# Optimization experiments

Hardware: AMD Instinct MI355X
Metric: run time of the kernel (lower is better)

The kernel has to match this reference:

```python
import jax, jax.numpy as jnp
import numpy as np

N = 50000      # nodes
E = 400000     # edges (before self-loops)
G = 256        # graphs in batch
H = 2          # attention heads
C = 100        # out channels per head
F_IN = 336
SLOPE = 0.2    # PyG GATConv default negative_slope


def setup_inputs() -> dict:
    key = jax.random.key(0)
    ks = jax.random.split(key, 32)
    inp = {}
    inp['x'] = jax.random.normal(ks[0], (N, F_IN), dtype=jnp.float32)
    inp['edge_index'] = jax.random.randint(ks[1], (2, E), 0, N, dtype=jnp.int32)
    inp['batch'] = jnp.sort(jax.random.randint(ks[2], (N,), 0, G, dtype=jnp.int32))
    dims = [F_IN, 200, 200, 200, 200]
    k = 3
    for i in range(5):
        d = dims[i]
        inp[f'W{i+1}'] = jax.random.normal(ks[k], (d, H * C), dtype=jnp.float32) / float(np.sqrt(d)); k += 1
        inp[f'asrc{i+1}'] = jax.random.normal(ks[k], (H, C), dtype=jnp.float32) * 0.1; k += 1
        inp[f'adst{i+1}'] = jax.random.normal(ks[k], (H, C), dtype=jnp.float32) * 0.1; k += 1
        inp[f'bc{i+1}'] = jnp.zeros((H * C,), jnp.float32)
    for i, (a, b) in enumerate([(200, 100), (100, 100), (100, 29)]):
        inp[f'lw{i+1}'] = jax.random.normal(ks[k], (a, b), dtype=jnp.float32) / float(np.sqrt(a)); k += 1
        inp[f'lb{i+1}'] = jnp.zeros((b,), jnp.float32)
    return inp


def _gat(x, src, dst, W, a_s, a_d, b):
    # PyG GATConv (concat=True): per-head linear, additive attention,
    # softmax over incoming edges per destination node, weighted sum.
    h = (x @ W).reshape(-1, H, C)                      # [N,H,C]
    es = jnp.einsum('nhc,hc->nh', h, a_s)              # [N,H] src scores
    ed = jnp.einsum('nhc,hc->nh', h, a_d)              # [N,H] dst scores
    e = jax.nn.leaky_relu(es[src] + ed[dst], SLOPE)    # [E+N,H]
    m = jax.ops.segment_max(e, dst, num_segments=N)    # per-dest max (stable softmax)
    p = jnp.exp(e - m[dst])
    s = jax.ops.segment_sum(p, dst, num_segments=N)
    alpha = p / (s[dst] + 1e-16)                       # [E+N,H]
    msg = alpha[:, :, None] * h[src]                   # [E+N,H,C]
    out = jax.ops.segment_sum(msg, dst, num_segments=N)
    return out.reshape(-1, H * C) + b


def reference(x, edge_index, batch,
              W1, asrc1, adst1, bc1, W2, asrc2, adst2, bc2,
              W3, asrc3, adst3, bc3, W4, asrc4, adst4, bc4,
              W5, asrc5, adst5, bc5,
              lw1, lb1, lw2, lb2, lw3, lb3):
    loop = jnp.arange(N, dtype=edge_index.dtype)       # self-loops (PyG default)
    src = jnp.concatenate([edge_index[0], loop])
    dst = jnp.concatenate([edge_index[1], loop])
    for W, a_s, a_d, b in [(W1, asrc1, adst1, bc1), (W2, asrc2, adst2, bc2),
                           (W3, asrc3, adst3, bc3), (W4, asrc4, adst4, bc4),
                           (W5, asrc5, adst5, bc5)]:
        x = jax.nn.relu(_gat(x, src, dst, W, a_s, a_d, b))
    # global mean pool over nodes of each graph
    sums = jax.ops.segment_sum(x, batch, num_segments=G)
    cnt = jax.ops.segment_sum(jnp.ones((N, 1), x.dtype), batch, num_segments=G)
    x = sums / jnp.maximum(cnt, 1.0)
    x = jax.nn.relu(x @ lw1 + lb1)
    x = jax.nn.relu(x @ lw2 + lb2)
    return x @ lw3 + lb3
```

## Files before the change

kernel.cpp:

```cpp
#include <hip/hip_runtime.h>
#include <hip/hip_bf16.h>
#include <math.h>

#define F_IN   336
#define HC     200
#define Cch    100
#define SLOPE  0.2f
#define SCAN_BS 256

#define NPAD   224
#define KP0    352
#define KP1    224

using short8   = __attribute__((ext_vector_type(8))) short;
using float4v  = __attribute__((ext_vector_type(4))) float;
using ushort4v = __attribute__((ext_vector_type(4))) unsigned short;
using float2v  = __attribute__((ext_vector_type(2))) float;

__device__ inline unsigned short rne_bf16(float v) {
    unsigned int u = __float_as_uint(v);
    return (unsigned short)((u + 0x7fffu + ((u >> 16) & 1u)) >> 16);
}
__device__ inline void split_bf(float v, unsigned short& hi, unsigned short& lo) {
    hi = rne_bf16(v);
    float hv = __uint_as_float(((unsigned int)hi) << 16);
    lo = rne_bf16(v - hv);
}

__global__ void init_deg(int* deg, int n) {
    int i = blockIdx.x * 256 + threadIdx.x;
    if (i < n) deg[i] = 1;
}

__global__ void count_deg(const int* __restrict__ dst, int* deg, int e) {
    int i = blockIdx.x * 256 + threadIdx.x;
    if (i < e) atomicAdd(&deg[dst[i]], 1);
}

__global__ void scan_block(const int* __restrict__ deg, int* incl, int* bsums, int n) {
    __shared__ int sm[SCAN_BS];
    int i = blockIdx.x * SCAN_BS + threadIdx.x;
    int v = (i < n) ? deg[i] : 0;
    sm[threadIdx.x] = v;
    __syncthreads();
    for (int off = 1; off < SCAN_BS; off <<= 1) {
        int t = (threadIdx.x >= off) ? sm[threadIdx.x - off] : 0;
        __syncthreads();
        sm[threadIdx.x] += t;
        __syncthreads();
    }
    if (i < n) incl[i] = sm[threadIdx.x];
    if (threadIdx.x == SCAN_BS - 1) bsums[blockIdx.x] = sm[threadIdx.x];
}

__global__ void scan_sums(int* bsums, int nb) {
    __shared__ int sm[SCAN_BS];
    int v = (threadIdx.x < nb) ? bsums[threadIdx.x] : 0;
    sm[threadIdx.x] = v;
    __syncthreads();
    for (int off = 1; off < SCAN_BS; off <<= 1) {
        int t = (threadIdx.x >= off) ? sm[threadIdx.x - off] : 0;
        __syncthreads();
        sm[threadIdx.x] += t;
        __syncthreads();
    }
    if (threadIdx.x < nb) bsums[threadIdx.x] = sm[threadIdx.x] - v;
}

__global__ void scan_final(const int* __restrict__ incl, const int* __restrict__ deg,
                           const int* __restrict__ bsums, int* row_ptr, int* cursor, int n) {
    int i = blockIdx.x * SCAN_BS + threadIdx.x;
    if (i < n) {
        int inc = incl[i] + bsums[i / SCAN_BS];
        int ex  = inc - deg[i];
        row_ptr[i] = ex;
        cursor[i]  = ex;
        if (i == n - 1) row_ptr[n] = inc;
    }
}

__global__ void fill_csr(const int* __restrict__ src, const int* __restrict__ dst,
                         int* cursor, int* col_src, int e, int n) {
    int i = blockIdx.x * 256 + threadIdx.x;
    int te = e + n;
    if (i >= te) return;
    int s, d;
    if (i < e) { s = src[i]; d = dst[i]; }
    else       { s = i - e;  d = i - e; }
    int pos = atomicAdd(&cursor[d], 1);
    col_src[pos] = s;
}

__global__ void conv_x(const float* __restrict__ x, unsigned short* __restrict__ Ah,
                       unsigned short* __restrict__ Al, int n_nodes) {
    const int GPR = KP0 / 4;
    int i = blockIdx.x * 256 + threadIdx.x;
    int tot = n_nodes * GPR;
    if (i >= tot) return;
    int row = i / GPR, g4 = i - row * GPR;
    int col = g4 * 4;
    float4v v = {0.f, 0.f, 0.f, 0.f};
    if (col < F_IN) v = *(const float4v*)(x + (size_t)row * F_IN + col);
    ushort4v hv, lv;
    split_bf(v.x, ((unsigned short*)&hv)[0], ((unsigned short*)&lv)[0]);
    split_bf(v.y, ((unsigned short*)&hv)[1], ((unsigned short*)&lv)[1]);
    split_bf(v.z, ((unsigned short*)&hv)[2], ((unsigned short*)&lv)[2]);
    split_bf(v.w, ((unsigned short*)&hv)[3], ((unsigned short*)&lv)[3]);
    size_t b = (size_t)row * KP0 + col;
    *(ushort4v*)(Ah + b) = hv;
    *(ushort4v*)(Al + b) = lv;
}

__global__ void conv_w(const float* __restrict__ W, unsigned short* __restrict__ Bh,
                       unsigned short* __restrict__ Bl, int K, int Kp) {
    int i = blockIdx.x * 256 + threadIdx.x;
    int tot = NPAD * Kp;
    if (i >= tot) return;
    int n = i / Kp, k = i - n * Kp;
    float v = (n < HC && k < K) ? W[(size_t)k * HC + n] : 0.f;
    unsigned short hi, lo;
    split_bf(v, hi, lo);
    Bh[i] = hi; Bl[i] = lo;
}

#define LDK 40
__global__ __launch_bounds__(256, 2) void gemm_split(
    const unsigned short* __restrict__ Ah, const unsigned short* __restrict__ Al,
    const unsigned short* __restrict__ Bh, const unsigned short* __restrict__ Bl,
    const float* __restrict__ asrc, const float* __restrict__ adst,
    float* __restrict__ h, float* __restrict__ es, float* __restrict__ ed,
    int M, int Kp)
{
    __shared__ unsigned short As[2][64][LDK];
    __shared__ unsigned short Bs[2][NPAD][LDK];
    __shared__ float sc[64][4];
    int tid  = threadIdx.x;
    int wave = tid >> 6, lane = tid & 63;
    int quad = lane >> 4, l16 = lane & 15;
    int wm = (wave >> 1) * 32;
    int wn = (wave & 1) * 112;
    int r0 = blockIdx.x * 64;

    ((float*)sc)[tid] = 0.f;

    float4v acc[2][7];
#pragma unroll
    for (int mt = 0; mt < 2; mt++)
#pragma unroll
        for (int nt = 0; nt < 7; nt++)
            acc[mt][nt] = (float4v){0.f, 0.f, 0.f, 0.f};

    for (int k0 = 0; k0 < Kp; k0 += 32) {
#pragma unroll
        for (int i = 0; i < 2; i++) {
            int c = tid + 256 * i;
            int s = c >> 8;
            int cc = c & 255;
            int row = cc >> 2, kc = (cc & 3) * 8;
            const unsigned short* g = s ? Al : Ah;
            uint4 v = make_uint4(0u, 0u, 0u, 0u);
            int gr = r0 + row;
            if (gr < M) v = *(const uint4*)(g + (size_t)gr * Kp + k0 + kc);
            *(uint4*)&As[s][row][kc] = v;
        }
#pragma unroll
        for (int i = 0; i < 7; i++) {
            int c = tid + 256 * i;
            int s = (c >= 896) ? 1 : 0;
            int cc = c - s * 896;
            int row = cc >> 2, kc = (cc & 3) * 8;
            const unsigned short* g = s ? Bl : Bh;
            *(uint4*)&Bs[s][row][kc] = *(const uint4*)(g + (size_t)row * Kp + k0 + kc);
        }
        __syncthreads();

        short8 a_h[2], a_l[2];
#pragma unroll
        for (int mt = 0; mt < 2; mt++) {
            a_h[mt] = *(const short8*)&As[0][wm + mt * 16 + l16][quad * 8];
            a_l[mt] = *(const short8*)&As[1][wm + mt * 16 + l16][quad * 8];
        }
#pragma unroll
        for (int nt = 0; nt < 7; nt++) {
            short8 b_h = *(const short8*)&Bs[0][wn + nt * 16 + l16][quad * 8];
            short8 b_l = *(const short8*)&Bs[1][wn + nt * 16 + l16][quad * 8];
#pragma unroll
            for (int mt = 0; mt < 2; mt++) {
                acc[mt][nt] = __builtin_amdgcn_mfma_f32_16x16x32_bf16(a_h[mt], b_h, acc[mt][nt], 0, 0, 0);
                acc[mt][nt] = __builtin_amdgcn_mfma_f32_16x16x32_bf16(a_h[mt], b_l, acc[mt][nt], 0, 0, 0);
                acc[mt][nt] = __builtin_amdgcn_mfma_f32_16x16x32_bf16(a_l[mt], b_h, acc[mt][nt], 0, 0, 0);
            }
        }
        __syncthreads();
    }

    float asc[7], adc[7];
    bool  vld[7];
    bool  hd1[7];
#pragma unroll
    for (int nt = 0; nt < 7; nt++) {
        int col = wn + nt * 16 + l16;
        vld[nt] = col < HC;
        hd1[nt] = col >= Cch;
        asc[nt] = vld[nt] ? asrc[col] : 0.f;
        adc[nt] = vld[nt] ? adst[col] : 0.f;
    }

#pragma unroll
    for (int mt = 0; mt < 2; mt++) {
        float p[4][4];
#pragma unroll
        for (int r = 0; r < 4; r++)
#pragma unroll
            for (int t = 0; t < 4; t++) p[r][t] = 0.f;
#pragma unroll
        for (int nt = 0; nt < 7; nt++) {
            int col = wn + nt * 16 + l16;
#pragma unroll
            for (int r = 0; r < 4; r++) {
                float v = acc[mt][nt][r];
                int grow = r0 + wm + mt * 16 + quad * 4 + r;
                if (vld[nt] && grow < M) h[(size_t)grow * HC + col] = v;
                float va = v * asc[nt], vd = v * adc[nt];
                p[r][0] += hd1[nt] ? 0.f : va;
                p[r][1] += hd1[nt] ? va  : 0.f;
                p[r][2] += hd1[nt] ? 0.f : vd;
                p[r][3] += hd1[nt] ? vd  : 0.f;
            }
        }
#pragma unroll
        for (int off = 1; off < 16; off <<= 1)
#pragma unroll
            for (int r = 0; r < 4; r++)
#pragma unroll
                for (int t = 0; t < 4; t++)
                    p[r][t] += __shfl_xor(p[r][t], off);
        if (l16 == 0) {
            int lrow = wm + mt * 16 + quad * 4;
#pragma unroll
            for (int r = 0; r < 4; r++)
#pragma unroll
                for (int t = 0; t < 4; t++)
                    atomicAdd(&sc[lrow + r][t], p[r][t]);
        }
    }
    __syncthreads();
    if (tid < 64) {
        int grow = r0 + tid;
        if (grow < M) {
            es[grow * 2 + 0] = sc[tid][0];
            es[grow * 2 + 1] = sc[tid][1];
            ed[grow * 2 + 0] = sc[tid][2];
            ed[grow * 2 + 1] = sc[tid][3];
        }
    }
}

__global__ __launch_bounds__(256) void gat_alpha_par(
    const float* __restrict__ es, const float* __restrict__ ed,
    const int* __restrict__ row_ptr, const int* __restrict__ col_src,
    float* __restrict__ pbuf, float* __restrict__ linv, int n_nodes)
{
    int tid = threadIdx.x;
    int sub = tid >> 4;
    int l   = tid & 15;
    int n = blockIdx.x * 16 + sub;
    if (n >= n_nodes) return;
    int e0 = row_ptr[n], e1 = row_ptr[n + 1];
    float ed0 = ed[n * 2], ed1 = ed[n * 2 + 1];
    float m0 = -INFINITY, m1 = -INFINITY;
    for (int e = e0 + l; e < e1; e += 16) {
        int s = col_src[e];
        float2v q = *(const float2v*)&es[s * 2];
        float s0 = q.x + ed0, s1 = q.y + ed1;
        s0 = s0 > 0.f ? s0 : SLOPE * s0;
        s1 = s1 > 0.f ? s1 : SLOPE * s1;
        m0 = fmaxf(m0, s0); m1 = fmaxf(m1, s1);
        float2v w = {s0, s1};
        *(float2v*)&pbuf[(size_t)e * 2] = w;
    }
#pragma unroll
    for (int off = 1; off < 16; off <<= 1) {
        m0 = fmaxf(m0, __shfl_xor(m0, off));
        m1 = fmaxf(m1, __shfl_xor(m1, off));
    }
    float l0 = 0.f, l1 = 0.f;
    for (int e = e0 + l; e < e1; e += 16) {
        float2v w = *(const float2v*)&pbuf[(size_t)e * 2];
        float p0 = __expf(w.x - m0), p1 = __expf(w.y - m1);
        l0 += p0; l1 += p1;
        float2v pp = {p0, p1};
        *(float2v*)&pbuf[(size_t)e * 2] = pp;
    }
#pragma unroll
    for (int off = 1; off < 16; off <<= 1) {
        l0 += __shfl_xor(l0, off);
        l1 += __shfl_xor(l1, off);
    }
    if (l == 0) {
        linv[n * 2]     = 1.f / (l0 + 1e-16f);
        linv[n * 2 + 1] = 1.f / (l1 + 1e-16f);
    }
}

template<bool WF, bool WB>
__global__ __launch_bounds__(256) void gat_gather(
    const float* __restrict__ h, const float* __restrict__ pbuf, const float* __restrict__ linv,
    const int* __restrict__ row_ptr, const int* __restrict__ col_src,
    const float* __restrict__ bias, float* __restrict__ outF,
    unsigned short* __restrict__ oh, unsigned short* __restrict__ ol, int n_nodes)
{
    int wave = threadIdx.x >> 6, lane = threadIdx.x & 63;
    int n = blockIdx.x * 4 + wave;
    if (n >= n_nodes) return;
    int e0 = row_ptr[n], e1 = row_ptr[n + 1];
    bool act  = lane < 50;
    int  hsel = (lane >= 25) ? 1 : 0;

    float4v a0 = {0.f, 0.f, 0.f, 0.f}, a1 = {0.f, 0.f, 0.f, 0.f};
    float4v a2 = {0.f, 0.f, 0.f, 0.f}, a3 = {0.f, 0.f, 0.f, 0.f};

    for (int cbase = e0; cbase < e1; cbase += 64) {
        int cnt = e1 - cbase; if (cnt > 64) cnt = 64;
        int   sidx = 0;
        float px = 0.f, py = 0.f;
        if (lane < cnt) {
            sidx = col_src[cbase + lane];
            float2v pp = *(const float2v*)&pbuf[(size_t)(cbase + lane) * 2];
            px = pp.x; py = pp.y;
        }
        int j = 0;
        for (; j + 4 <= cnt; j += 4) {
            int s0 = __shfl(sidx, j + 0), s1 = __shfl(sidx, j + 1);
            int s2 = __shfl(sidx, j + 2), s3 = __shfl(sidx, j + 3);
            float x0 = __shfl(px, j + 0), y0 = __shfl(py, j + 0);
            float x1 = __shfl(px, j + 1), y1 = __shfl(py, j + 1);
            float x2 = __shfl(px, j + 2), y2 = __shfl(py, j + 2);
            float x3 = __shfl(px, j + 3), y3 = __shfl(py, j + 3);
            float p0 = hsel ? y0 : x0;
            float p1 = hsel ? y1 : x1;
            float p2 = hsel ? y2 : x2;
            float p3 = hsel ? y3 : x3;
            if (act) {
                float4v v0 = *(const float4v*)(h + (size_t)s0 * HC + lane * 4);
                float4v v1 = *(const float4v*)(h + (size_t)s1 * HC + lane * 4);
                float4v v2 = *(const float4v*)(h + (size_t)s2 * HC + lane * 4);
                float4v v3 = *(const float4v*)(h + (size_t)s3 * HC + lane * 4);
                a0.x += p0 * v0.x; a0.y += p0 * v0.y; a0.z += p0 * v0.z; a0.w += p0 * v0.w;
                a1.x += p1 * v1.x; a1.y += p1 * v1.y; a1.z += p1 * v1.z; a1.w += p1 * v1.w;
                a2.x += p2 * v2.x; a2.y += p2 * v2.y; a2.z += p2 * v2.z; a2.w += p2 * v2.w;
                a3.x += p3 * v3.x; a3.y += p3 * v3.y; a3.z += p3 * v3.z; a3.w += p3 * v3.w;
            }
        }
        for (; j < cnt; j++) {
            int s0 = __shfl(sidx, j);
            float x0 = __shfl(px, j), y0 = __shfl(py, j);
            float p0 = hsel ? y0 : x0;
            if (act) {
                float4v v0 = *(const float4v*)(h + (size_t)s0 * HC + lane * 4);
                a0.x += p0 * v0.x; a0.y += p0 * v0.y; a0.z += p0 * v0.z; a0.w += p0 * v0.w;
            }
        }
    }
    float4v acc;
    acc.x = (a0.x + a1.x) + (a2.x + a3.x);
    acc.y = (a0.y + a1.y) + (a2.y + a3.y);
    acc.z = (a0.z + a1.z) + (a2.z + a3.z);
    acc.w = (a0.w + a1.w) + (a2.w + a3.w);

    float li = linv[n * 2 + hsel];
    if (act) {
        float4v bb = *(const float4v*)(bias + lane * 4);
        float4v r;
        r.x = fmaxf(acc.x * li + bb.x, 0.f);
        r.y = fmaxf(acc.y * li + bb.y, 0.f);
        r.z = fmaxf(acc.z * li + bb.z, 0.f);
        r.w = fmaxf(acc.w * li + bb.w, 0.f);
        if (WF) {
            __builtin_nontemporal_store(r, (float4v*)(outF + (size_t)n * HC + lane * 4));
        }
        if (WB) {
            ushort4v hv, lv;
            split_bf(r.x, ((unsigned short*)&hv)[0], ((unsigned short*)&lv)[0]);
            split_bf(r.y, ((unsigned short*)&hv)[1], ((unsigned short*)&lv)[1]);
            split_bf(r.z, ((unsigned short*)&hv)[2], ((unsigned short*)&lv)[2]);
            split_bf(r.w, ((unsigned short*)&hv)[3], ((unsigned short*)&lv)[3]);
            size_t b = (size_t)n * NPAD + lane * 4;
            __builtin_nontemporal_store(hv, (ushort4v*)(oh + b));
            __builtin_nontemporal_store(lv, (ushort4v*)(ol + b));
        }
    } else if (WB && lane < 56) {
        ushort4v z = {0, 0, 0, 0};
        size_t b = (size_t)n * NPAD + lane * 4;
        __builtin_nontemporal_store(z, (ushort4v*)(oh + b));
        __builtin_nontemporal_store(z, (ushort4v*)(ol + b));
    }
}

__global__ void pool_zero(float* pool, int tot) {
    int i = blockIdx.x * 256 + threadIdx.x;
    if (i < tot) pool[i] = 0.f;
}

__global__ __launch_bounds__(256) void pool_part(
    const float* __restrict__ x, const int* __restrict__ batch,
    float* __restrict__ pool, int n_nodes)
{
    int wave = threadIdx.x >> 6, lane = threadIdx.x & 63;
    int base = (blockIdx.x * 4 + wave) * 16;
    if (base >= n_nodes) return;
    bool act = lane < 50;
    int end = base + 16; if (end > n_nodes) end = n_nodes;
    float4v acc = {0.f, 0.f, 0.f, 0.f};
    int curg = batch[base];
    for (int n = base; n < end; n++) {
        int g = batch[n];
        if (g != curg) {
            if (act) {
                float* pp = pool + (size_t)curg * HC + lane * 4;
                atomicAdd(pp + 0, acc.x); atomicAdd(pp + 1, acc.y);
                atomicAdd(pp + 2, acc.z); atomicAdd(pp + 3, acc.w);
            }
            acc = (float4v){0.f, 0.f, 0.f, 0.f};
            curg = g;
        }
        if (act) {
            float4v v = *(const float4v*)(x + (size_t)n * HC + lane * 4);
            acc.x += v.x; acc.y += v.y; acc.z += v.z; acc.w += v.w;
        }
    }
    if (act) {
        float* pp = pool + (size_t)curg * HC + lane * 4;
        atomicAdd(pp + 0, acc.x); atomicAdd(pp + 1, acc.y);
        atomicAdd(pp + 2, acc.z); atomicAdd(pp + 3, acc.w);
    }
}

__global__ void pool_div(float* pool, const int* __restrict__ gstart, int g_count) {
    int i = blockIdx.x * 256 + threadIdx.x;
    if (i >= g_count * HC) return;
    int g = i / HC;
    float cnt = (float)(gstart[g + 1] - gstart[g]);
    pool[i] /= fmaxf(cnt, 1.f);
}

__global__ void graph_bounds(const int* __restrict__ batch, int* gstart, int n, int g) {
    int i = blockIdx.x * 256 + threadIdx.x;
    if (i >= n) return;
    int b = batch[i];
    int bp = (i == 0) ? -1 : batch[i - 1];
    for (int q = bp + 1; q <= b; q++) gstart[q] = i;
    if (i == n - 1) for (int q = b + 1; q <= g; q++) gstart[q] = n;
}

template<int KIN, int KOUT, bool RELU>
__global__ __launch_bounds__(128) void mlp(
    const float* __restrict__ in, const float* __restrict__ W, const float* __restrict__ b,
    float* __restrict__ out)
{
    __shared__ float xi[KIN];
    int g = blockIdx.x;
    for (int k = threadIdx.x; k < KIN; k += blockDim.x) xi[k] = in[g * KIN + k];
    __syncthreads();
    int j = threadIdx.x;
    if (j < KOUT) {
        float s = b[j];
        for (int k = 0; k < KIN; k++) s = fmaf(xi[k], W[k * KOUT + j], s);
        if (RELU) s = fmaxf(s, 0.f);
        out[g * KOUT + j] = s;
    }
}

extern "C" void kernel_launch(void* const* d_in, const int* in_sizes, int n_in,
                              void* d_out, int out_size, void* d_ws, size_t ws_size,
                              hipStream_t stream) {
    const float* x     = (const float*)d_in[0];
    const int*   ei    = (const int*)d_in[1];
    const int*   batch = (const int*)d_in[2];
    const float *W[5], *asrc[5], *adst[5], *bc[5];
    for (int i = 0; i < 5; i++) {
        W[i]    = (const float*)d_in[3 + i * 4];
        asrc[i] = (const float*)d_in[4 + i * 4];
        adst[i] = (const float*)d_in[5 + i * 4];
        bc[i]   = (const float*)d_in[6 + i * 4];
    }
    const float* lw1 = (const float*)d_in[23];
    const float* lb1 = (const float*)d_in[24];
    const float* lw2 = (const float*)d_in[25];
    const float* lb2 = (const float*)d_in[26];
    const float* lw3 = (const float*)d_in[27];
    const float* lb3 = (const float*)d_in[28];
    float* out = (float*)d_out;

    const int N  = in_sizes[0] / F_IN;
    const int E  = in_sizes[1] / 2;
    const int G  = out_size / 29;
    const int TE = E + N;
    const int* esrc = ei;
    const int* edst = ei + E;

    char* p = (char*)d_ws;
    auto carve = [&](size_t bytes) { void* r = (void*)p; p += ((bytes + 255) / 256) * 256; return r; };
    float*          hbuf = (float*)carve((size_t)N * HC * 4);
    unsigned short* Ah   = (unsigned short*)carve((size_t)N * KP0 * 2);
    unsigned short* Al   = (unsigned short*)carve((size_t)N * KP0 * 2);
    float*          outF = (float*)Ah;
    unsigned short* Wth  = (unsigned short*)carve((size_t)NPAD * KP0 * 2);
    unsigned short* Wtl  = (unsigned short*)carve((size_t)NPAD * KP0 * 2);
    float* es_     = (float*)carve((size_t)N * 2 * 4);
    float* ed_     = (float*)carve((size_t)N * 2 * 4);
    float* pbuf    = (float*)carve((size_t)TE * 2 * 4);
    float* linv    = (float*)carve((size_t)N * 2 * 4);
    int*   deg     = (int*)carve((size_t)N * 4);
    int*   incl    = (int*)carve((size_t)N * 4);
    int*   bsums   = (int*)carve(SCAN_BS * 4);
    int*   row_ptr = (int*)carve((size_t)(N + 1) * 4);
    int*   cursor  = (int*)carve((size_t)N * 4);
    int*   col_src = (int*)carve((size_t)TE * 4);
    int*   gstart  = (int*)carve((size_t)(G + 1) * 4);
    float* pool    = (float*)carve((size_t)G * HC * 4);
    float* t1      = (float*)carve((size_t)G * 100 * 4);
    float* t2      = (float*)carve((size_t)G * 100 * 4);

    const int nBlkN   = (N + 255) / 256;
    const int nBlkE   = (E + 255) / 256;
    const int nBlkTE  = (TE + 255) / 256;
    const int nScanB  = (N + SCAN_BS - 1) / SCAN_BS;
    const int nWaveB  = (N + 3) / 4;
    const int nGemmB  = (N + 63) / 64;
    const int nPoolB  = (N + 63) / 64;
    const int nAlphaB = (N + 15) / 16;

    init_deg<<<nBlkN, 256, 0, stream>>>(deg, N);
    count_deg<<<nBlkE, 256, 0, stream>>>(edst, deg, E);
    scan_block<<<nScanB, SCAN_BS, 0, stream>>>(deg, incl, bsums, N);
    scan_sums<<<1, SCAN_BS, 0, stream>>>(bsums, nScanB);
    scan_final<<<nScanB, SCAN_BS, 0, stream>>>(incl, deg, bsums, row_ptr, cursor, N);
    fill_csr<<<nBlkTE, 256, 0, stream>>>(esrc, edst, cursor, col_src, E, N);

    conv_x<<<(N * (KP0 / 4) + 255) / 256, 256, 0, stream>>>(x, Ah, Al, N);

    for (int L = 0; L < 5; L++) {
        int K  = (L == 0) ? F_IN : HC;
        int Kp = (L == 0) ? KP0 : KP1;
        conv_w<<<(NPAD * Kp + 255) / 256, 256, 0, stream>>>(W[L], Wth, Wtl, K, Kp);
        gemm_split<<<nGemmB, 256, 0, stream>>>(Ah, Al, Wth, Wtl, asrc[L], adst[L],
                                               hbuf, es_, ed_, N, Kp);
        gat_alpha_par<<<nAlphaB, 256, 0, stream>>>(es_, ed_, row_ptr, col_src, pbuf, linv, N);
        if (L < 4)
            gat_gather<false, true><<<nWaveB, 256, 0, stream>>>(hbuf, pbuf, linv, row_ptr, col_src,
                                                                bc[L], nullptr, Ah, Al, N);
        else
            gat_gather<true, false><<<nWaveB, 256, 0, stream>>>(hbuf, pbuf, linv, row_ptr, col_src,
                                                                bc[L], outF, nullptr, nullptr, N);
    }

    graph_bounds<<<nBlkN, 256, 0, stream>>>(batch, gstart, N, G);
    pool_zero<<<(G * HC + 255) / 256, 256, 0, stream>>>(pool, G * HC);
    pool_part<<<nPoolB, 256, 0, stream>>>(outF, batch, pool, N);
    pool_div<<<(G * HC + 255) / 256, 256, 0, stream>>>(pool, gstart, G);

    mlp<200, 100, true ><<<G, 128, 0, stream>>>(pool, lw1, lb1, t1);
    mlp<100, 100, true ><<<G, 128, 0, stream>>>(t1, lw2, lb2, t2);
    mlp<100, 29,  false><<<G, 128, 0, stream>>>(t2, lw3, lb3, out);
}
```

Before: 834.8 us.

## Load GEMM MFMA operands directly from global memory, skipping LDS staging

The split-bf16 GEMM no longer stages A and B tiles through shared memory. Each lane now loads its MFMA fragments straight from global memory using precomputed row pointers. The K dimension becomes a template parameter so the k-loop fully unrolls, and occupancy is raised to 3 blocks per CU. This removes LDS traffic and two barriers per k-step, but each wave re-reads B (weights) from global/L2 with no cross-wave sharing and issues less-coalesced 16-byte loads.

```diff
diff --git a/kernel.cpp b/kernel.cpp
--- a/kernel.cpp
+++ b/kernel.cpp
@@ -123,16 +123,14 @@
     Bh[i] = hi; Bl[i] = lo;
 }
 
-#define LDK 40
-__global__ __launch_bounds__(256, 2) void gemm_split(
+template<int KP>
+__global__ __launch_bounds__(256, 3) void gemm_direct(
     const unsigned short* __restrict__ Ah, const unsigned short* __restrict__ Al,
     const unsigned short* __restrict__ Bh, const unsigned short* __restrict__ Bl,
     const float* __restrict__ asrc, const float* __restrict__ adst,
     float* __restrict__ h, float* __restrict__ es, float* __restrict__ ed,
-    int M, int Kp)
+    int M)
 {
-    __shared__ unsigned short As[2][64][LDK];
-    __shared__ unsigned short Bs[2][NPAD][LDK];
     __shared__ float sc[64][4];
     int tid  = threadIdx.x;
     int wave = tid >> 6, lane = tid & 63;
@@ -142,6 +140,28 @@
     int r0 = blockIdx.x * 64;
 
     ((float*)sc)[tid] = 0.f;
+    __syncthreads();
+
+    int  arow[2];
+    bool avld[2];
+    const unsigned short* pa_h[2];
+    const unsigned short* pa_l[2];
+#pragma unroll
+    for (int mt = 0; mt < 2; mt++) {
+        arow[mt] = r0 + wm + mt * 16 + l16;
+        avld[mt] = arow[mt] < M;
+        size_t off = (size_t)(avld[mt] ? arow[mt] : 0) * KP + quad * 8;
+        pa_h[mt] = Ah + off;
+        pa_l[mt] = Al + off;
+    }
+    const unsigned short* pb_h[7];
+    const unsigned short* pb_l[7];
+#pragma unroll
+    for (int nt = 0; nt < 7; nt++) {
+        size_t off = (size_t)(wn + nt * 16 + l16) * KP + quad * 8;
+        pb_h[nt] = Bh + off;
+        pb_l[nt] = Bl + off;
+    }
 
     float4v acc[2][7];
 #pragma unroll
@@ -150,40 +170,19 @@
         for (int nt = 0; nt < 7; nt++)
             acc[mt][nt] = (float4v){0.f, 0.f, 0.f, 0.f};
 
-    for (int k0 = 0; k0 < Kp; k0 += 32) {
-#pragma unroll
-        for (int i = 0; i < 2; i++) {
-            int c = tid + 256 * i;
-            int s = c >> 8;
-            int cc = c & 255;
-            int row = cc >> 2, kc = (cc & 3) * 8;
-            const unsigned short* g = s ? Al : Ah;
-            uint4 v = make_uint4(0u, 0u, 0u, 0u);
-            int gr = r0 + row;
-            if (gr < M) v = *(const uint4*)(g + (size_t)gr * Kp + k0 + kc);
-            *(uint4*)&As[s][row][kc] = v;
-        }
-#pragma unroll
-        for (int i = 0; i < 7; i++) {
-            int c = tid + 256 * i;
-            int s = (c >= 896) ? 1 : 0;
-            int cc = c - s * 896;
-            int row = cc >> 2, kc = (cc & 3) * 8;
-            const unsigned short* g = s ? Bl : Bh;
-            *(uint4*)&Bs[s][row][kc] = *(const uint4*)(g + (size_t)row * Kp + k0 + kc);
-        }
-        __syncthreads();
-
+    const short8 zero8 = {0, 0, 0, 0, 0, 0, 0, 0};
+#pragma unroll
+    for (int k0 = 0; k0 < KP; k0 += 32) {
         short8 a_h[2], a_l[2];
 #pragma unroll
         for (int mt = 0; mt < 2; mt++) {
-            a_h[mt] = *(const short8*)&As[0][wm + mt * 16 + l16][quad * 8];
-            a_l[mt] = *(const short8*)&As[1][wm + mt * 16 + l16][quad * 8];
+            a_h[mt] = avld[mt] ? *(const short8*)(pa_h[mt] + k0) : zero8;
+            a_l[mt] = avld[mt] ? *(const short8*)(pa_l[mt] + k0) : zero8;
         }
 #pragma unroll
         for (int nt = 0; nt < 7; nt++) {
-            short8 b_h = *(const short8*)&Bs[0][wn + nt * 16 + l16][quad * 8];
-            short8 b_l = *(const short8*)&Bs[1][wn + nt * 16 + l16][quad * 8];
+            short8 b_h = *(const short8*)(pb_h[nt] + k0);
+            short8 b_l = *(const short8*)(pb_l[nt] + k0);
 #pragma unroll
             for (int mt = 0; mt < 2; mt++) {
                 acc[mt][nt] = __builtin_amdgcn_mfma_f32_16x16x32_bf16(a_h[mt], b_h, acc[mt][nt], 0, 0, 0);
@@ -191,7 +190,6 @@
                 acc[mt][nt] = __builtin_amdgcn_mfma_f32_16x16x32_bf16(a_l[mt], b_h, acc[mt][nt], 0, 0, 0);
             }
         }
-        __syncthreads();
     }
 
     float asc[7], adc[7];
@@ -544,8 +542,12 @@
         int K  = (L == 0) ? F_IN : HC;
         int Kp = (L == 0) ? KP0 : KP1;
         conv_w<<<(NPAD * Kp + 255) / 256, 256, 0, stream>>>(W[L], Wth, Wtl, K, Kp);
-        gemm_split<<<nGemmB, 256, 0, stream>>>(Ah, Al, Wth, Wtl, asrc[L], adst[L],
-                                               hbuf, es_, ed_, N, Kp);
+        if (L == 0)
+            gemm_direct<KP0><<<nGemmB, 256, 0, stream>>>(Ah, Al, Wth, Wtl, asrc[L], adst[L],
+                                                         hbuf, es_, ed_, N);
+        else
+            gemm_direct<KP1><<<nGemmB, 256, 0, stream>>>(Ah, Al, Wth, Wtl, asrc[L], adst[L],
+                                                         hbuf, es_, ed_, N);
         gat_alpha_par<<<nAlphaB, 256, 0, stream>>>(es_, ed_, row_ptr, col_src, pbuf, linv, N);
         if (L < 4)
             gat_gather<false, true><<<nWaveB, 256, 0, stream>>>(hbuf, pbuf, linv, row_ptr, col_src,
```

New measurement: 925.3 us. 10.8% more time.
